# Performance work log

Measured on AMD Instinct MI355X. Metric: run time of the kernel, lower is better.

## Reference

```python
import jax, jax.numpy as jnp
import numpy as np

DIM = 768
HEADS = 12
HEAD_DIM = DIM // HEADS
HIDDEN = 4 * DIM
SCALE = HEAD_DIM ** -0.5
LN_EPS = 1e-5


def _fit_poly_gelu():
    # replicate PolyGELU.__init__: quadratic least-squares fit to exact GELU on [-3,3]
    x = np.linspace(-3.0, 3.0, 10000).astype(np.float32)
    y = np.asarray(jax.nn.gelu(jnp.asarray(x), approximate=False))
    X = np.stack([x ** 2, x, np.ones_like(x)], axis=1)
    c, *_ = np.linalg.lstsq(X, y, rcond=None)
    return c.astype(np.float32)  # [a, b, c]


def setup_inputs() -> dict:
    key = jax.random.key(0)
    ks = jax.random.split(key, 8)
    g = _fit_poly_gelu()
    w = lambda k, shp: (jax.random.normal(k, shp, dtype=jnp.float32) * 0.02)
    return {
        "x": jax.random.normal(ks[0], (4, 2048, DIM), dtype=jnp.float32),
        "ln1_g": jnp.ones((DIM,), jnp.float32),
        "ln1_b": jnp.zeros((DIM,), jnp.float32),
        "ln2_g": jnp.ones((DIM,), jnp.float32),
        "ln2_b": jnp.zeros((DIM,), jnp.float32),
        "qkv_w": w(ks[1], (DIM, 3 * DIM)),   # stored [in, out]
        "qkv_b": jnp.zeros((3 * DIM,), jnp.float32),
        "proj_w": w(ks[2], (DIM, DIM)),
        "proj_b": jnp.zeros((DIM,), jnp.float32),
        "fc1_w": w(ks[3], (DIM, HIDDEN)),
        "fc1_b": jnp.zeros((HIDDEN,), jnp.float32),
        "fc2_w": w(ks[4], (HIDDEN, DIM)),
        "fc2_b": jnp.zeros((DIM,), jnp.float32),
        "attn_a": jnp.float32(0.05),
        "attn_b": jnp.float32(0.5),
        "attn_c": jnp.float32(0.25),
        "gelu_a": jnp.float32(g[0]),
        "gelu_b": jnp.float32(g[1]),
        "gelu_c": jnp.float32(g[2]),
    }


def _layernorm(x, gamma, beta):
    mu = jnp.mean(x, axis=-1, keepdims=True)
    var = jnp.mean(jnp.square(x - mu), axis=-1, keepdims=True)
    return (x - mu) / jnp.sqrt(var + LN_EPS) * gamma + beta


def reference(x, ln1_g, ln1_b, ln2_g, ln2_b, qkv_w, qkv_b, proj_w, proj_b,
              fc1_w, fc1_b, fc2_w, fc2_b, attn_a, attn_b, attn_c,
              gelu_a, gelu_b, gelu_c):
    B, N, C = x.shape
    # --- attention branch ---
    h = _layernorm(x, ln1_g, ln1_b)
    qkv = (h @ qkv_w + qkv_b).reshape(B, N, 3, HEADS, HEAD_DIM)
    q, k, v = (qkv[:, :, i].transpose(0, 2, 1, 3) for i in range(3))  # [B,H,N,D]
    attn = jnp.einsum("bhnd,bhmd->bhnm", q, k) * SCALE
    # poly_normed: quadratic activation, clamp, row-normalize
    attn = attn_a * attn * attn + attn_b * attn + attn_c
    attn = jnp.maximum(attn, 1e-6)
    attn = attn / (jnp.sum(attn, axis=-1, keepdims=True) + 1e-8)
    out = jnp.einsum("bhnm,bhmd->bhnd", attn, v).transpose(0, 2, 1, 3).reshape(B, N, C)
    x = x + (out @ proj_w + proj_b)
    # --- MLP branch with PolyGELU ---
    h = _layernorm(x, ln2_g, ln2_b)
    u = h @ fc1_w + fc1_b
    u = gelu_a * u * u + gelu_b * u + gelu_c
    x = x + (u @ fc2_w + fc2_b)
    return x
```

## Files before the change

### kernel.cpp

```cpp
#include <hip/hip_runtime.h>

typedef __bf16 bf16x8 __attribute__((ext_vector_type(8)));
typedef __bf16 bf16x4 __attribute__((ext_vector_type(4)));
typedef float f32x4 __attribute__((ext_vector_type(4)));

#define LN_EPS 1e-5f

__device__ __forceinline__ void gl2lds16(const void* g, void* l) {
  __builtin_amdgcn_global_load_lds(
      (const __attribute__((address_space(1))) unsigned int*)g,
      (__attribute__((address_space(3))) unsigned int*)l, 16, 0, 0);
}

__global__ __launch_bounds__(256) void transpose_k(const float* __restrict__ in,
                                                   __bf16* __restrict__ out,
                                                   int R, int C) {
  __shared__ __bf16 t[32][33];
  int tx = threadIdx.x & 31, ty = threadIdx.x >> 5;
  int c = blockIdx.x * 32 + tx;
  for (int j = 0; j < 4; j++) {
    int r = blockIdx.y * 32 + ty + j * 8;
    t[ty + j * 8][tx] = (__bf16)in[(size_t)r * C + c];
  }
  __syncthreads();
  int r2 = blockIdx.y * 32 + tx;
  for (int j = 0; j < 4; j++) {
    int c2 = blockIdx.x * 32 + ty + j * 8;
    out[(size_t)c2 * R + r2] = t[tx][ty + j * 8];
  }
}

__global__ __launch_bounds__(256) void transpose_v(const __bf16* __restrict__ qkv,
                                                   __bf16* __restrict__ vt) {
  __shared__ __bf16 t[32][33];
  int bh = blockIdx.z;
  int b = bh / 12, h = bh % 12;
  int n0 = blockIdx.x * 32, d0 = blockIdx.y * 32;
  int tx = threadIdx.x & 31, ty = threadIdx.x >> 5;
  for (int j = 0; j < 4; j++) {
    int n = n0 + ty + j * 8;
    t[ty + j * 8][tx] = qkv[(size_t)(b * 2048 + n) * 2304 + 1536 + h * 64 + d0 + tx];
  }
  __syncthreads();
  for (int j = 0; j < 4; j++) {
    int d = d0 + ty + j * 8;
    vt[((size_t)bh * 64 + d) * 2048 + n0 + tx] = t[tx][ty + j * 8];
  }
}

__global__ __launch_bounds__(256) void ln_kernel(const float* __restrict__ x,
                                                 const float* __restrict__ g,
                                                 const float* __restrict__ bta,
                                                 __bf16* __restrict__ out) {
  int row = blockIdx.x;
  size_t base = (size_t)row * 768;
  int t = threadIdx.x;
  float v[3];
  float s = 0.f, s2 = 0.f;
  for (int k = 0; k < 3; k++) {
    float f = x[base + t + k * 256];
    v[k] = f;
    s += f;
    s2 += f * f;
  }
  for (int m = 1; m < 64; m <<= 1) {
    s += __shfl_xor(s, m, 64);
    s2 += __shfl_xor(s2, m, 64);
  }
  __shared__ float sm[4][2];
  int wid = t >> 6, lane = t & 63;
  if (lane == 0) { sm[wid][0] = s; sm[wid][1] = s2; }
  __syncthreads();
  s = sm[0][0] + sm[1][0] + sm[2][0] + sm[3][0];
  s2 = sm[0][1] + sm[1][1] + sm[2][1] + sm[3][1];
  float mu = s * (1.f / 768.f);
  float var = s2 * (1.f / 768.f) - mu * mu;
  float rstd = rsqrtf(var + LN_EPS);
  for (int k = 0; k < 3; k++) {
    int c = t + k * 256;
    out[base + c] = (__bf16)((v[k] - mu) * rstd * g[c] + bta[c]);
  }
}

template <int EPI>
__global__ __launch_bounds__(256) void gemm128(const __bf16* __restrict__ A,
                                               const __bf16* __restrict__ BT,
                                               const float* __restrict__ bias,
                                               const float* __restrict__ res,
                                               void* __restrict__ outv,
                                               int M, int N, int K,
                                               const float* __restrict__ c0p,
                                               const float* __restrict__ c1p,
                                               const float* __restrict__ c2p) {
  __shared__ __bf16 As[128][32];
  __shared__ __bf16 Bs[128][32];
  int tid = threadIdx.x;
  int lane = tid & 63, wid = tid >> 6;
  int wr = wid >> 1, wc = wid & 1;
  int m0 = blockIdx.y * 128, n0 = blockIdx.x * 128;
  int mr = lane & 15, kq = (lane >> 4) * 8;
  int srow = tid >> 2, scol = (tid & 3) * 8;

  f32x4 acc[4][4] = {};

  for (int k0 = 0; k0 < K; k0 += 32) {
    for (int i = 0; i < 2; i++) {
      int row = srow + i * 64;
      gl2lds16(&A[(size_t)(m0 + row) * K + k0 + scol], &As[row][scol]);
      gl2lds16(&BT[(size_t)(n0 + row) * K + k0 + scol], &Bs[row][scol]);
    }
    __syncthreads();
    bf16x8 af[4], bfr[4];
    for (int i = 0; i < 4; i++) af[i] = *(bf16x8*)&As[wr * 64 + i * 16 + mr][kq];
    for (int j = 0; j < 4; j++) bfr[j] = *(bf16x8*)&Bs[wc * 64 + j * 16 + mr][kq];
    for (int i = 0; i < 4; i++)
      for (int j = 0; j < 4; j++)
        acc[i][j] = __builtin_amdgcn_mfma_f32_16x16x32_bf16(af[i], bfr[j], acc[i][j], 0, 0, 0);
    __syncthreads();
  }

  float ga = 0.f, gb = 0.f, gc = 0.f;
  if (EPI == 1) { ga = *c0p; gb = *c1p; gc = *c2p; }

  for (int i = 0; i < 4; i++) {
    for (int j = 0; j < 4; j++) {
      int col = n0 + wc * 64 + j * 16 + mr;
      float bv = bias[col];
      for (int r = 0; r < 4; r++) {
        int row = m0 + wr * 64 + i * 16 + (lane >> 4) * 4 + r;
        size_t idx = (size_t)row * N + col;
        float c = acc[i][j][r] + bv;
        if (EPI == 0) {
          ((__bf16*)outv)[idx] = (__bf16)c;
        } else if (EPI == 1) {
          float u = (ga * c + gb) * c + gc;
          ((__bf16*)outv)[idx] = (__bf16)u;
        } else {
          ((float*)outv)[idx] = c + res[idx];
        }
      }
    }
  }
}

__global__ __launch_bounds__(256, 4) void attn_poly(const __bf16* __restrict__ qkv,
                                                    const __bf16* __restrict__ vt,
                                                    __bf16* __restrict__ outp,
                                                    const float* __restrict__ ap,
                                                    const float* __restrict__ bp,
                                                    const float* __restrict__ cp) {
  __shared__ __bf16 QPs[4][32][72];
  __shared__ __bf16 Ks[64][72];
  __shared__ __bf16 Vts[64][72];
  __bf16(*Qs)[72] = (__bf16(*)[72]) & QPs[0][0][0];

  int tid = threadIdx.x, lane = tid & 63, wid = tid >> 6;
  int mr = lane & 15, quad = lane >> 4, kq = quad * 8;
  int q0 = blockIdx.x * 128;
  int h = blockIdx.y, b = blockIdx.z;
  int bh = b * 12 + h;
  size_t baseQ = ((size_t)b * 2048) * 2304 + h * 64;

  for (int i = 0; i < 4; i++) {
    int chunk = tid + i * 256;
    int row = chunk >> 3, dc = chunk & 7;
    *(bf16x8*)&Qs[row][dc * 8] =
        *(const bf16x8*)&qkv[baseQ + (size_t)(q0 + row) * 2304 + dc * 8];
  }
  __syncthreads();

  bf16x8 qf[2][2];
  for (int i = 0; i < 2; i++)
    for (int s = 0; s < 2; s++)
      qf[i][s] = *(bf16x8*)&Qs[wid * 32 + i * 16 + mr][s * 32 + kq];

  float a2 = (*ap) * 0.015625f, b2 = (*bp) * 0.125f, cc = *cp;
  f32x4 o_acc[2][4] = {};
  float l_acc[2] = {0.f, 0.f};

  for (int kt = 0; kt < 32; kt++) {
    __syncthreads();
    for (int i = 0; i < 2; i++) {
      int chunk = tid + i * 256;
      int row = chunk >> 3, dc = chunk & 7;
      *(bf16x8*)&Ks[row][dc * 8] =
          *(const bf16x8*)&qkv[baseQ + (size_t)(kt * 64 + row) * 2304 + 768 + dc * 8];
      *(bf16x8*)&Vts[row][dc * 8] =
          *(const bf16x8*)&vt[((size_t)bh * 64 + row) * 2048 + kt * 64 + dc * 8];
    }
    __syncthreads();

    bf16x8 kf[4][2];
    for (int j = 0; j < 4; j++)
      for (int s = 0; s < 2; s++)
        kf[j][s] = *(bf16x8*)&Ks[j * 16 + mr][s * 32 + kq];

    for (int i = 0; i < 2; i++) {
      f32x4 sacc[4] = {};
      for (int j = 0; j < 4; j++)
        for (int s = 0; s < 2; s++)
          sacc[j] = __builtin_amdgcn_mfma_f32_16x16x32_bf16(kf[j][s], qf[i][s], sacc[j], 0, 0, 0);
      float rsum = 0.f;
      for (int j = 0; j < 4; j++) {
        bf16x4 pk;
        for (int r = 0; r < 4; r++) {
          float S = sacc[j][r];
          float p = fmaf(fmaf(a2, S, b2), S, cc);
          p = fmaxf(p, 1e-6f);
          rsum += p;
          pk[r] = (__bf16)p;
        }
        *(bf16x4*)&QPs[wid][i * 16 + mr][j * 16 + quad * 4] = pk;
      }
      rsum += __shfl_xor(rsum, 16, 64);
      rsum += __shfl_xor(rsum, 32, 64);
      l_acc[i] += rsum;
    }

    __syncthreads();

    for (int i = 0; i < 2; i++) {
      for (int s = 0; s < 2; s++) {
        bf16x8 pf = *(bf16x8*)&QPs[wid][i * 16 + mr][s * 32 + kq];
        for (int dt = 0; dt < 4; dt++) {
          bf16x8 vf = *(bf16x8*)&Vts[dt * 16 + mr][s * 32 + kq];
          o_acc[i][dt] = __builtin_amdgcn_mfma_f32_16x16x32_bf16(pf, vf, o_acc[i][dt], 0, 0, 0);
        }
      }
    }
  }

  size_t baseO = ((size_t)b * 2048) * 768 + h * 64;
  for (int i = 0; i < 2; i++) {
    float inv[4];
    for (int r = 0; r < 4; r++)
      inv[r] = 1.0f / (__shfl(l_acc[i], quad * 4 + r, 64) + 1e-8f);
    for (int dt = 0; dt < 4; dt++) {
      int q = q0 + wid * 32 + i * 16 + quad * 4;
      for (int r = 0; r < 4; r++) {
        outp[baseO + (size_t)(q + r) * 768 + dt * 16 + mr] =
            (__bf16)(o_acc[i][dt][r] * inv[r]);
      }
    }
  }
}

extern "C" void kernel_launch(void* const* d_in, const int* in_sizes, int n_in,
                              void* d_out, int out_size, void* d_ws, size_t ws_size,
                              hipStream_t stream) {
  const float* x     = (const float*)d_in[0];
  const float* ln1g  = (const float*)d_in[1];
  const float* ln1b  = (const float*)d_in[2];
  const float* ln2g  = (const float*)d_in[3];
  const float* ln2b  = (const float*)d_in[4];
  const float* qkvw  = (const float*)d_in[5];
  const float* qkvb  = (const float*)d_in[6];
  const float* projw = (const float*)d_in[7];
  const float* projb = (const float*)d_in[8];
  const float* fc1w  = (const float*)d_in[9];
  const float* fc1b  = (const float*)d_in[10];
  const float* fc2w  = (const float*)d_in[11];
  const float* fc2b  = (const float*)d_in[12];
  const float* attna = (const float*)d_in[13];
  const float* attnb = (const float*)d_in[14];
  const float* attnc = (const float*)d_in[15];
  const float* gelua = (const float*)d_in[16];
  const float* gelub = (const float*)d_in[17];
  const float* geluc = (const float*)d_in[18];

  char* ws = (char*)d_ws;
  __bf16* wT_qkv  = (__bf16*)(ws);
  __bf16* wT_proj = (__bf16*)(ws + 3538944);
  __bf16* wT_fc1  = (__bf16*)(ws + 4718592);
  __bf16* wT_fc2  = (__bf16*)(ws + 9437184);
  __bf16* h       = (__bf16*)(ws + 14155776);
  float*  x1      = (float*)(ws + 26738688);
  __bf16* qkvbuf  = (__bf16*)(ws + 51904512);
  __bf16* u       = (__bf16*)(ws + 51904512);
  __bf16* vtbuf   = (__bf16*)(ws + 89653248);
  float*  outp    = (float*)d_out;

  transpose_k<<<dim3(2304 / 32, 768 / 32), 256, 0, stream>>>(qkvw, wT_qkv, 768, 2304);
  transpose_k<<<dim3(768 / 32, 768 / 32), 256, 0, stream>>>(projw, wT_proj, 768, 768);
  transpose_k<<<dim3(3072 / 32, 768 / 32), 256, 0, stream>>>(fc1w, wT_fc1, 768, 3072);
  transpose_k<<<dim3(768 / 32, 3072 / 32), 256, 0, stream>>>(fc2w, wT_fc2, 3072, 768);

  ln_kernel<<<8192, 256, 0, stream>>>(x, ln1g, ln1b, h);
  gemm128<0><<<dim3(18, 64), 256, 0, stream>>>(h, wT_qkv, qkvb, nullptr, qkvbuf,
                                               8192, 2304, 768, nullptr, nullptr, nullptr);
  transpose_v<<<dim3(64, 2, 48), 256, 0, stream>>>(qkvbuf, vtbuf);
  attn_poly<<<dim3(16, 12, 4), 256, 0, stream>>>(qkvbuf, vtbuf, h, attna, attnb, attnc);
  gemm128<2><<<dim3(6, 64), 256, 0, stream>>>(h, wT_proj, projb, x, x1,
                                              8192, 768, 768, nullptr, nullptr, nullptr);
  ln_kernel<<<8192, 256, 0, stream>>>(x1, ln2g, ln2b, h);
  gemm128<1><<<dim3(24, 64), 256, 0, stream>>>(h, wT_fc1, fc1b, nullptr, u,
                                               8192, 3072, 768, gelua, gelub, geluc);
  gemm128<2><<<dim3(6, 64), 256, 0, stream>>>(u, wT_fc2, fc2b, x1, outp,
                                              8192, 768, 3072, nullptr, nullptr, nullptr);
}
```

Measured before the change: 480.3 us.

## Use BK=64 swizzled GEMM tiles and double-buffered async K/V staging in attention

Replaces the GEMM with a BK=64 version that uses XOR-swizzled LDS layout and wider 128x256 tiles for the QKV and FC1 projections. This halves the K-loop barriers and is meant to reduce LDS bank conflicts. The attention kernel now loads Q straight into registers and double-buffers K/V tiles with async global-to-LDS loads, which removes one barrier per iteration and overlaps loads with compute. Launch bounds change as well, which reduces occupancy and raises register pressure.

```diff
diff --git a/kernel.cpp b/kernel.cpp
--- a/kernel.cpp
+++ b/kernel.cpp
@@ -82,40 +82,46 @@
   }
 }
 
-template <int EPI>
-__global__ __launch_bounds__(256) void gemm128(const __bf16* __restrict__ A,
-                                               const __bf16* __restrict__ BT,
-                                               const float* __restrict__ bias,
-                                               const float* __restrict__ res,
-                                               void* __restrict__ outv,
-                                               int M, int N, int K,
-                                               const float* __restrict__ c0p,
-                                               const float* __restrict__ c1p,
-                                               const float* __restrict__ c2p) {
-  __shared__ __bf16 As[128][32];
-  __shared__ __bf16 Bs[128][32];
-  int tid = threadIdx.x;
-  int lane = tid & 63, wid = tid >> 6;
-  int wr = wid >> 1, wc = wid & 1;
-  int m0 = blockIdx.y * 128, n0 = blockIdx.x * 128;
-  int mr = lane & 15, kq = (lane >> 4) * 8;
-  int srow = tid >> 2, scol = (tid & 3) * 8;
-
-  f32x4 acc[4][4] = {};
-
-  for (int k0 = 0; k0 < K; k0 += 32) {
-    for (int i = 0; i < 2; i++) {
-      int row = srow + i * 64;
-      gl2lds16(&A[(size_t)(m0 + row) * K + k0 + scol], &As[row][scol]);
-      gl2lds16(&BT[(size_t)(n0 + row) * K + k0 + scol], &Bs[row][scol]);
+template <int NT, int EPI>
+__global__ __launch_bounds__(256, (NT == 128 ? 3 : 2))
+void gemm_bk64(const __bf16* __restrict__ A, const __bf16* __restrict__ BT,
+               const float* __restrict__ bias, const float* __restrict__ res,
+               void* __restrict__ outv, int M, int N, int K,
+               const float* __restrict__ c0p, const float* __restrict__ c1p,
+               const float* __restrict__ c2p) {
+  __shared__ __bf16 As[128][64];
+  __shared__ __bf16 Bs[NT][64];
+  const int tid = threadIdx.x, lane = tid & 63, wid = tid >> 6;
+  const int wr = wid >> 1, wc = wid & 1;
+  const int mr = lane & 15, quad = lane >> 4;
+  const int m0 = blockIdx.y * 128, n0 = blockIdx.x * NT;
+  const int swzsrc = (((lane & 7) ^ ((lane >> 3) & 7)) * 8);
+  const int srow8 = lane >> 3;
+  const int col0 = ((quad ^ (mr & 7)) * 8);
+  const int col1 = (((4 + quad) ^ (mr & 7)) * 8);
+
+  f32x4 acc[4][NT / 32] = {};
+
+  for (int k0 = 0; k0 < K; k0 += 64) {
+    for (int g = 0; g < 4; g++) {
+      int r0 = wid * 32 + g * 8 + srow8;
+      gl2lds16(&A[(size_t)(m0 + r0) * K + k0 + swzsrc], &As[r0][(lane & 7) * 8]);
+    }
+    for (int g = 0; g < NT / 32; g++) {
+      int r0 = wid * (NT / 4) + g * 8 + srow8;
+      gl2lds16(&BT[(size_t)(n0 + r0) * K + k0 + swzsrc], &Bs[r0][(lane & 7) * 8]);
     }
     __syncthreads();
-    bf16x8 af[4], bfr[4];
-    for (int i = 0; i < 4; i++) af[i] = *(bf16x8*)&As[wr * 64 + i * 16 + mr][kq];
-    for (int j = 0; j < 4; j++) bfr[j] = *(bf16x8*)&Bs[wc * 64 + j * 16 + mr][kq];
-    for (int i = 0; i < 4; i++)
-      for (int j = 0; j < 4; j++)
-        acc[i][j] = __builtin_amdgcn_mfma_f32_16x16x32_bf16(af[i], bfr[j], acc[i][j], 0, 0, 0);
+    for (int kk = 0; kk < 2; kk++) {
+      const int ck = kk ? col1 : col0;
+      bf16x8 af[4], bfr[NT / 32];
+      for (int i = 0; i < 4; i++) af[i] = *(bf16x8*)&As[wr * 64 + i * 16 + mr][ck];
+      for (int j = 0; j < NT / 32; j++)
+        bfr[j] = *(bf16x8*)&Bs[wc * (NT / 2) + j * 16 + mr][ck];
+      for (int i = 0; i < 4; i++)
+        for (int j = 0; j < NT / 32; j++)
+          acc[i][j] = __builtin_amdgcn_mfma_f32_16x16x32_bf16(af[i], bfr[j], acc[i][j], 0, 0, 0);
+    }
     __syncthreads();
   }
 
@@ -123,11 +129,11 @@
   if (EPI == 1) { ga = *c0p; gb = *c1p; gc = *c2p; }
 
   for (int i = 0; i < 4; i++) {
-    for (int j = 0; j < 4; j++) {
-      int col = n0 + wc * 64 + j * 16 + mr;
+    for (int j = 0; j < NT / 32; j++) {
+      int col = n0 + wc * (NT / 2) + j * 16 + mr;
       float bv = bias[col];
       for (int r = 0; r < 4; r++) {
-        int row = m0 + wr * 64 + i * 16 + (lane >> 4) * 4 + r;
+        int row = m0 + wr * 64 + i * 16 + quad * 4 + r;
         size_t idx = (size_t)row * N + col;
         float c = acc[i][j][r] + bv;
         if (EPI == 0) {
@@ -143,91 +149,93 @@
   }
 }
 
-__global__ __launch_bounds__(256, 4) void attn_poly(const __bf16* __restrict__ qkv,
+__global__ __launch_bounds__(256, 3) void attn_poly(const __bf16* __restrict__ qkv,
                                                     const __bf16* __restrict__ vt,
                                                     __bf16* __restrict__ outp,
                                                     const float* __restrict__ ap,
                                                     const float* __restrict__ bp,
                                                     const float* __restrict__ cp) {
-  __shared__ __bf16 QPs[4][32][72];
-  __shared__ __bf16 Ks[64][72];
-  __shared__ __bf16 Vts[64][72];
-  __bf16(*Qs)[72] = (__bf16(*)[72]) & QPs[0][0][0];
-
-  int tid = threadIdx.x, lane = tid & 63, wid = tid >> 6;
-  int mr = lane & 15, quad = lane >> 4, kq = quad * 8;
-  int q0 = blockIdx.x * 128;
-  int h = blockIdx.y, b = blockIdx.z;
-  int bh = b * 12 + h;
-  size_t baseQ = ((size_t)b * 2048) * 2304 + h * 64;
-
-  for (int i = 0; i < 4; i++) {
-    int chunk = tid + i * 256;
-    int row = chunk >> 3, dc = chunk & 7;
-    *(bf16x8*)&Qs[row][dc * 8] =
-        *(const bf16x8*)&qkv[baseQ + (size_t)(q0 + row) * 2304 + dc * 8];
-  }
-  __syncthreads();
+  __shared__ __bf16 Ps[4][32][72];
+  __shared__ __bf16 Kb[2][64][64];
+  __shared__ __bf16 Vb[2][64][64];
+
+  const int tid = threadIdx.x, lane = tid & 63, wid = tid >> 6;
+  const int mr = lane & 15, quad = lane >> 4;
+  const int q0 = blockIdx.x * 128;
+  const int h = blockIdx.y, b = blockIdx.z;
+  const int bh = b * 12 + h;
+  const size_t baseQ = ((size_t)b * 2048) * 2304 + h * 64;
+
+  const int swzsrc = (((lane & 7) ^ ((lane >> 3) & 7)) * 8);
+  const int srow8 = lane >> 3;
+  const int colS0 = ((quad ^ (mr & 7)) * 8);
+  const int colS1 = (((4 + quad) ^ (mr & 7)) * 8);
 
   bf16x8 qf[2][2];
   for (int i = 0; i < 2; i++)
     for (int s = 0; s < 2; s++)
-      qf[i][s] = *(bf16x8*)&Qs[wid * 32 + i * 16 + mr][s * 32 + kq];
-
-  float a2 = (*ap) * 0.015625f, b2 = (*bp) * 0.125f, cc = *cp;
+      qf[i][s] = *(const bf16x8*)&qkv[baseQ + (size_t)(q0 + wid * 32 + i * 16 + mr) * 2304 +
+                                      s * 32 + quad * 8];
+
+  const float a2 = (*ap) * 0.015625f, b2 = (*bp) * 0.125f, cc = *cp;
   f32x4 o_acc[2][4] = {};
   float l_acc[2] = {0.f, 0.f};
 
+  auto stage = [&](int kt, int pb) {
+    for (int g = 0; g < 2; g++) {
+      int r0 = wid * 16 + g * 8 + srow8;
+      gl2lds16(&qkv[baseQ + (size_t)(kt * 64 + r0) * 2304 + 768 + swzsrc],
+               &Kb[pb][r0][(lane & 7) * 8]);
+      gl2lds16(&vt[((size_t)bh * 64 + r0) * 2048 + kt * 64 + swzsrc],
+               &Vb[pb][r0][(lane & 7) * 8]);
+    }
+  };
+
+  stage(0, 0);
+  int pb = 0;
   for (int kt = 0; kt < 32; kt++) {
     __syncthreads();
+    if (kt < 31) stage(kt + 1, pb ^ 1);
+
+    f32x4 sacc[2][4] = {};
+    for (int j = 0; j < 4; j++) {
+      for (int s = 0; s < 2; s++) {
+        bf16x8 kf = *(bf16x8*)&Kb[pb][j * 16 + mr][s ? colS1 : colS0];
+        for (int i = 0; i < 2; i++)
+          sacc[i][j] = __builtin_amdgcn_mfma_f32_16x16x32_bf16(kf, qf[i][s], sacc[i][j], 0, 0, 0);
+      }
+    }
     for (int i = 0; i < 2; i++) {
-      int chunk = tid + i * 256;
-      int row = chunk >> 3, dc = chunk & 7;
-      *(bf16x8*)&Ks[row][dc * 8] =
-          *(const bf16x8*)&qkv[baseQ + (size_t)(kt * 64 + row) * 2304 + 768 + dc * 8];
-      *(bf16x8*)&Vts[row][dc * 8] =
-          *(const bf16x8*)&vt[((size_t)bh * 64 + row) * 2048 + kt * 64 + dc * 8];
-    }
-    __syncthreads();
-
-    bf16x8 kf[4][2];
-    for (int j = 0; j < 4; j++)
-      for (int s = 0; s < 2; s++)
-        kf[j][s] = *(bf16x8*)&Ks[j * 16 + mr][s * 32 + kq];
-
-    for (int i = 0; i < 2; i++) {
-      f32x4 sacc[4] = {};
-      for (int j = 0; j < 4; j++)
-        for (int s = 0; s < 2; s++)
-          sacc[j] = __builtin_amdgcn_mfma_f32_16x16x32_bf16(kf[j][s], qf[i][s], sacc[j], 0, 0, 0);
-      float rsum = 0.f;
+      f32x4 racc = {0.f, 0.f, 0.f, 0.f};
       for (int j = 0; j < 4; j++) {
-        bf16x4 pk;
-        for (int r = 0; r < 4; r++) {
-          float S = sacc[j][r];
-          float p = fmaf(fmaf(a2, S, b2), S, cc);
-          p = fmaxf(p, 1e-6f);
-          rsum += p;
-          pk[r] = (__bf16)p;
-        }
-        *(bf16x4*)&QPs[wid][i * 16 + mr][j * 16 + quad * 4] = pk;
+        f32x4 S = sacc[i][j];
+        f32x4 p = (a2 * S + b2) * S + cc;
+        p[0] = fmaxf(p[0], 1e-6f); p[1] = fmaxf(p[1], 1e-6f);
+        p[2] = fmaxf(p[2], 1e-6f); p[3] = fmaxf(p[3], 1e-6f);
+        racc += p;
+        bf16x4 pk = {(__bf16)p[0], (__bf16)p[1], (__bf16)p[2], (__bf16)p[3]};
+        *(bf16x4*)&Ps[wid][i * 16 + mr][j * 16 + quad * 4] = pk;
       }
+      float rsum = racc[0] + racc[1] + racc[2] + racc[3];
       rsum += __shfl_xor(rsum, 16, 64);
       rsum += __shfl_xor(rsum, 32, 64);
       l_acc[i] += rsum;
     }
 
-    __syncthreads();
-
-    for (int i = 0; i < 2; i++) {
-      for (int s = 0; s < 2; s++) {
-        bf16x8 pf = *(bf16x8*)&QPs[wid][i * 16 + mr][s * 32 + kq];
-        for (int dt = 0; dt < 4; dt++) {
-          bf16x8 vf = *(bf16x8*)&Vts[dt * 16 + mr][s * 32 + kq];
-          o_acc[i][dt] = __builtin_amdgcn_mfma_f32_16x16x32_bf16(pf, vf, o_acc[i][dt], 0, 0, 0);
-        }
+    __asm__ __volatile__("s_waitcnt lgkmcnt(0)" ::: "memory");
+
+    for (int s = 0; s < 2; s++) {
+      bf16x8 pf[2];
+      for (int i = 0; i < 2; i++)
+        pf[i] = *(bf16x8*)&Ps[wid][i * 16 + mr][s * 32 + quad * 8];
+      for (int dt = 0; dt < 4; dt++) {
+        bf16x8 vf = *(bf16x8*)&Vb[pb][dt * 16 + mr][s ? colS1 : colS0];
+        for (int i = 0; i < 2; i++)
+          o_acc[i][dt] = __builtin_amdgcn_mfma_f32_16x16x32_bf16(pf[i], vf, o_acc[i][dt], 0, 0, 0);
       }
     }
+    __asm__ __volatile__("" ::: "memory");
+    pb ^= 1;
   }
 
   size_t baseO = ((size_t)b * 2048) * 768 + h * 64;
@@ -237,10 +245,9 @@
       inv[r] = 1.0f / (__shfl(l_acc[i], quad * 4 + r, 64) + 1e-8f);
     for (int dt = 0; dt < 4; dt++) {
       int q = q0 + wid * 32 + i * 16 + quad * 4;
-      for (int r = 0; r < 4; r++) {
+      for (int r = 0; r < 4; r++)
         outp[baseO + (size_t)(q + r) * 768 + dt * 16 + mr] =
             (__bf16)(o_acc[i][dt][r] * inv[r]);
-      }
     }
   }
 }
@@ -286,15 +293,15 @@
   transpose_k<<<dim3(768 / 32, 3072 / 32), 256, 0, stream>>>(fc2w, wT_fc2, 3072, 768);
 
   ln_kernel<<<8192, 256, 0, stream>>>(x, ln1g, ln1b, h);
-  gemm128<0><<<dim3(18, 64), 256, 0, stream>>>(h, wT_qkv, qkvb, nullptr, qkvbuf,
-                                               8192, 2304, 768, nullptr, nullptr, nullptr);
+  gemm_bk64<256, 0><<<dim3(9, 64), 256, 0, stream>>>(h, wT_qkv, qkvb, nullptr, qkvbuf,
+                                                     8192, 2304, 768, nullptr, nullptr, nullptr);
   transpose_v<<<dim3(64, 2, 48), 256, 0, stream>>>(qkvbuf, vtbuf);
   attn_poly<<<dim3(16, 12, 4), 256, 0, stream>>>(qkvbuf, vtbuf, h, attna, attnb, attnc);
-  gemm128<2><<<dim3(6, 64), 256, 0, stream>>>(h, wT_proj, projb, x, x1,
-                                              8192, 768, 768, nullptr, nullptr, nullptr);
+  gemm_bk64<128, 2><<<dim3(6, 64), 256, 0, stream>>>(h, wT_proj, projb, x, x1,
+                                                     8192, 768, 768, nullptr, nullptr, nullptr);
   ln_kernel<<<8192, 256, 0, stream>>>(x1, ln2g, ln2b, h);
-  gemm128<1><<<dim3(24, 64), 256, 0, stream>>>(h, wT_fc1, fc1b, nullptr, u,
-                                               8192, 3072, 768, gelua, gelub, geluc);
-  gemm128<2><<<dim3(6, 64), 256, 0, stream>>>(u, wT_fc2, fc2b, x1, outp,
-                                              8192, 768, 3072, nullptr, nullptr, nullptr);
-}
+  gemm_bk64<256, 1><<<dim3(12, 64), 256, 0, stream>>>(h, wT_fc1, fc1b, nullptr, u,
+                                                      8192, 3072, 768, gelua, gelub, geluc);
+  gemm_bk64<128, 2><<<dim3(6, 64), 256, 0, stream>>>(u, wT_fc2, fc2b, x1, outp,
+                                                     8192, 768, 3072, nullptr, nullptr, nullptr);
+}
```

Result: faster. 411.3 us (-14.4%).
